# Optimization experiments

Measured on AMD Instinct MI355X. Metric: run time of the kernel, lower is better.

## Reference

```python
import jax, jax.numpy as jnp
import numpy as np

STRIDE = (1, 1)
PAD = 1


def _conv2d(x, w):
    # NCHW conv, OIHW kernel, stride 1, padding 1 (module defaults)
    return jax.lax.conv_general_dilated(
        x, w, window_strides=STRIDE, padding=[(PAD, PAD), (PAD, PAD)],
        dimension_numbers=("NCHW", "OIHW", "NCHW"))


def setup_inputs() -> dict:
    key = jax.random.key(0)
    k1, k2, k3 = jax.random.split(key, 3)
    C, H, W, O, KH, KW = 16, 16, 16, 32, 3, 3
    N = C * H * W  # 4096 flat input features
    base = jax.random.normal(k1, (1, N), dtype=jnp.float32)
    return {
        "x": base,
        "lower_bound": base - 0.1,
        "upper_bound": base + 0.1,
        "input_shape": jnp.array([1, C, H, W], dtype=jnp.int32),
        "kernel": 0.1 * jax.random.normal(k2, (O, C, KH, KW), dtype=jnp.float32),
        "bias": 0.1 * jax.random.normal(k3, (O,), dtype=jnp.float32),
    }


def reference(x, lower_bound, upper_bound, input_shape, kernel, bias):
    shape = tuple(int(s) for s in np.asarray(input_shape))  # (1, C, H, W)
    x4 = x.reshape(shape)
    lb4 = lower_bound.reshape(shape)
    ub4 = upper_bound.reshape(shape)

    # twice inside F.conv2d and once via the explicit reshape-add)
    neg_w = jnp.where(kernel < 0, kernel, 0.0)
    pos_w = jnp.where(kernel >= 0, kernel, 0.0)
    b3 = (3.0 * bias)[None, :, None, None]
    lb_new = _conv2d(ub4, neg_w) + _conv2d(lb4, pos_w) + b3
    ub_new = _conv2d(lb4, neg_w) + _conv2d(ub4, pos_w) + b3
    lb_new = lb_new.reshape(lb_new.shape[0], -1)
    ub_new = ub_new.reshape(ub_new.shape[0], -1)

    # concrete forward through the conv layer (bias once)
    x_out4 = _conv2d(x4, kernel) + bias[None, :, None, None]
    x_out = x_out4.reshape(x_out4.shape[0], -1)

    # unroll conv into an explicit [numel_in, numel_out] matrix.
    # Equivalent to the source's eye().view + conv3d(depth-1 kernel):
    # each basis image is convolved independently -> batched conv2d.
    N = x.shape[1]
    eye_imgs = jnp.eye(N, dtype=kernel.dtype).reshape((N,) + shape[1:])  # [N,C,H,W]
    unrolled = _conv2d(eye_imgs, kernel)  # [N, O, H', W']
    weights = unrolled.reshape(N, -1)     # [numel_in, O*H'*W']
    O_, Hp, Wp = unrolled.shape[1:]
    bias_vec = jnp.broadcast_to(bias[:, None, None], (O_, Hp, Wp)).reshape(-1)

    return (x_out, lb_new, ub_new, weights, bias_vec)
```

## Files before the change

### kernel.cpp

```cpp
#include <hip/hip_runtime.h>

#define O_CH  32
#define C_CH  16
#define HH    16
#define WW    16
#define NPIX  256
#define NIN   4096
#define NOUT  8192
#define NB_WEIGHTS 2048
#define NB_BOUNDS  32

typedef float v4f __attribute__((ext_vector_type(4)));


__global__ __launch_bounds__(256) void fused_deeppoly_kernel(
    const float* __restrict__ x,
    const float* __restrict__ lb,
    const float* __restrict__ ub,
    const float* __restrict__ wk,
    const float* __restrict__ bias,
    float* __restrict__ out) {
    const int b   = blockIdx.x;
    const int tid = threadIdx.x;

    if (b < NB_WEIGHTS) {
        const int colgroup = b & 7;
        const int rowset   = b >> 3;
        const int r   = colgroup * 256 + tid;
        const int o   = r >> 6;
        const int p   = r & 63;
        const int ph  = p >> 2;
        const int pw0 = (p & 3) << 2;
        const int c   = rowset >> 4;
        const int h   = rowset & 15;
        const int kh  = h - ph + 1;

        float k0 = 0.f, k1 = 0.f, k2 = 0.f;
        if ((unsigned)kh < 3u) {
            const float* kb = wk + ((o * C_CH + c) * 3 + kh) * 3;
            k0 = kb[0]; k1 = kb[1]; k2 = kb[2];
        }
        auto sel = [&](int kw) -> float {
            return kw == 0 ? k0 : (kw == 1 ? k1 : (kw == 2 ? k2 : 0.f));
        };

        v4f* wout = (v4f*)(out + 3 * NOUT);
        v4f* pptr = wout + (size_t)(rowset * 16) * 2048 + r;

        v4f v;
        v.x = sel(1 - pw0);
        v.y = sel(-pw0);
        v.z = sel(-1 - pw0);
        v.w = sel(-2 - pw0);
        #pragma unroll
        for (int j = 0; j < 16; ++j) {
            __builtin_nontemporal_store(v, pptr);
            pptr += 2048;
            v.w = v.z; v.z = v.y; v.y = v.x;
            v.x = sel(j + 2 - pw0);
        }
    } else {
        const int o  = b - NB_WEIGHTS;
        const int ph = tid >> 4, pw = tid & 15;
        const float* kb_base = wk + o * C_CH * 9;
        float xa = 0.f, la = 0.f, ua = 0.f;
        #pragma unroll
        for (int c = 0; c < C_CH; ++c) {
            #pragma unroll
            for (int kh = 0; kh < 3; ++kh) {
                int h = ph + kh - 1;
                if ((unsigned)h >= (unsigned)HH) continue;
                #pragma unroll
                for (int kw = 0; kw < 3; ++kw) {
                    int w = pw + kw - 1;
                    if ((unsigned)w >= (unsigned)WW) continue;
                    float k   = kb_base[c * 9 + kh * 3 + kw];
                    int   idx = c * NPIX + h * WW + w;
                    xa = fmaf(k, x[idx], xa);
                    float lv = lb[idx], uv = ub[idx];
                    la = fmaf(k, (k < 0.f) ? uv : lv, la);
                    ua = fmaf(k, (k < 0.f) ? lv : uv, ua);
                }
            }
        }
        const int   t  = o * 256 + tid;
        const float bv = bias[o];
        out[t]            = xa + bv;
        out[NOUT + t]     = la + 3.f * bv;
        out[2 * NOUT + t] = ua + 3.f * bv;
        out[(size_t)3 * NOUT + (size_t)NIN * NOUT + t] = bv;
    }
}

extern "C" void kernel_launch(void* const* d_in, const int* in_sizes, int n_in,
                              void* d_out, int out_size, void* d_ws, size_t ws_size,
                              hipStream_t stream) {
    const float* x    = (const float*)d_in[0];
    const float* lbp  = (const float*)d_in[1];
    const float* ubp  = (const float*)d_in[2];
    const float* wk   = (const float*)d_in[4];
    const float* bias = (const float*)d_in[5];

    fused_deeppoly_kernel<<<NB_WEIGHTS + NB_BOUNDS, 256, 0, stream>>>(
        x, lbp, ubp, wk, bias, (float*)d_out);
}
```

Baseline: 165.4 us.

## Remap weight-matrix writer so each block writes two contiguous output rows

Each weight block now covers two consecutive input rows (a contiguous 64KB span) instead of 16 rows strided by 2048 vectors for one column group. Each thread issues 16 coalesced vector stores of 4096-float rows and reloads kernel taps per output channel. Nontemporal stores are replaced by ordinary stores. The aim is a more sequential DRAM write pattern, at the cost of more kernel-weight loads per thread and possible cache pollution from normal stores.

```diff
diff --git a/kernel.cpp b/kernel.cpp
--- a/kernel.cpp
+++ b/kernel.cpp
@@ -12,7 +12,6 @@
 
 typedef float v4f __attribute__((ext_vector_type(4)));
 
-
 __global__ __launch_bounds__(256) void fused_deeppoly_kernel(
     const float* __restrict__ x,
     const float* __restrict__ lb,
@@ -24,40 +23,40 @@
     const int tid = threadIdx.x;
 
     if (b < NB_WEIGHTS) {
-        const int colgroup = b & 7;
-        const int rowset   = b >> 3;
-        const int r   = colgroup * 256 + tid;
-        const int o   = r >> 6;
-        const int p   = r & 63;
-        const int ph  = p >> 2;
-        const int pw0 = (p & 3) << 2;
-        const int c   = rowset >> 4;
-        const int h   = rowset & 15;
-        const int kh  = h - ph + 1;
+        const int n0   = 2 * b;
+        const int c    = n0 >> 8;
+        const int h    = (n0 >> 4) & 15;
+        const int w0   = n0 & 15;
+        const int ph   = (tid & 63) >> 2;
+        const int pw0  = (tid & 3) << 2;
+        const int osub = tid >> 6;
+        const int kh   = h - ph + 1;
+        const bool kvalid = (unsigned)kh < 3u;
+        const int  khc = kvalid ? kh : 0;
 
-        float k0 = 0.f, k1 = 0.f, k2 = 0.f;
-        if ((unsigned)kh < 3u) {
-            const float* kb = wk + ((o * C_CH + c) * 3 + kh) * 3;
-            k0 = kb[0]; k1 = kb[1]; k2 = kb[2];
-        }
-        auto sel = [&](int kw) -> float {
-            return kw == 0 ? k0 : (kw == 1 ? k1 : (kw == 2 ? k2 : 0.f));
-        };
+        v4f* p = (v4f*)(out + 3 * NOUT) + (size_t)b * 4096 + tid;
 
-        v4f* wout = (v4f*)(out + 3 * NOUT);
-        v4f* pptr = wout + (size_t)(rowset * 16) * 2048 + r;
-
-        v4f v;
-        v.x = sel(1 - pw0);
-        v.y = sel(-pw0);
-        v.z = sel(-1 - pw0);
-        v.w = sel(-2 - pw0);
         #pragma unroll
-        for (int j = 0; j < 16; ++j) {
-            __builtin_nontemporal_store(v, pptr);
-            pptr += 2048;
-            v.w = v.z; v.z = v.y; v.y = v.x;
-            v.x = sel(j + 2 - pw0);
+        for (int half = 0; half < 2; ++half) {
+            const int w   = w0 + half;
+            const int kw0 = w - pw0 + 1;
+            #pragma unroll
+            for (int jj = 0; jj < 8; ++jj) {
+                const int o = jj * 4 + osub;
+                const float* kb = wk + ((o * C_CH + c) * 3 + khc) * 3;
+                float k0 = kb[0], k1 = kb[1], k2 = kb[2];
+                if (!kvalid) { k0 = 0.f; k1 = 0.f; k2 = 0.f; }
+                auto sel = [&](int kw) -> float {
+                    return kw == 0 ? k0 : (kw == 1 ? k1 : (kw == 2 ? k2 : 0.f));
+                };
+                v4f v;
+                v.x = sel(kw0);
+                v.y = sel(kw0 - 1);
+                v.z = sel(kw0 - 2);
+                v.w = sel(kw0 - 3);
+                *p = v;
+                p += 256;
+            }
         }
     } else {
         const int o  = b - NB_WEIGHTS;
```

Measured after the change: 163.5 us. Within noise of the previous version (-1.2%).

## Remap weight-matrix blocks by spatial position and loop over channels with plain stores

Applied to the files above, without the earlier changes.

The unrolled-weight writer now gives each block one (h,w) input position and loops over the 16 channels, each iteration reloading three kernel taps and writing a 16-byte vector with a stride of 524288 vec4s. The old version held one kernel row in registers and shifted it across 16 rows with nontemporal stores. Bounds blocks move to the front of the grid so they are scheduled first. The write pattern per block changes, each block now issues more small kernel loads, and the switch to normal stores may pollute the cache on this large write-only output.

```diff
diff --git a/kernel.cpp b/kernel.cpp
--- a/kernel.cpp
+++ b/kernel.cpp
@@ -7,11 +7,10 @@
 #define NPIX  256
 #define NIN   4096
 #define NOUT  8192
+#define NB_BOUNDS  32
 #define NB_WEIGHTS 2048
-#define NB_BOUNDS  32
 
 typedef float v4f __attribute__((ext_vector_type(4)));
-
 
 __global__ __launch_bounds__(256) void fused_deeppoly_kernel(
     const float* __restrict__ x,
@@ -23,44 +22,43 @@
     const int b   = blockIdx.x;
     const int tid = threadIdx.x;
 
-    if (b < NB_WEIGHTS) {
-        const int colgroup = b & 7;
-        const int rowset   = b >> 3;
-        const int r   = colgroup * 256 + tid;
+    if (b >= NB_BOUNDS) {
+        const int bw  = b - NB_BOUNDS;
+        const int nb  = bw >> 3;
+        const int r   = (bw & 7) * 256 + tid;
         const int o   = r >> 6;
         const int p   = r & 63;
         const int ph  = p >> 2;
         const int pw0 = (p & 3) << 2;
-        const int c   = rowset >> 4;
-        const int h   = rowset & 15;
+        const int h   = nb >> 4;
+        const int w   = nb & 15;
         const int kh  = h - ph + 1;
+        const bool kvalid = (unsigned)kh < 3u;
+        const int  khc = kvalid ? kh : 0;
+        const int  kw0 = w - pw0 + 1;
 
-        float k0 = 0.f, k1 = 0.f, k2 = 0.f;
-        if ((unsigned)kh < 3u) {
-            const float* kb = wk + ((o * C_CH + c) * 3 + kh) * 3;
-            k0 = kb[0]; k1 = kb[1]; k2 = kb[2];
-        }
-        auto sel = [&](int kw) -> float {
-            return kw == 0 ? k0 : (kw == 1 ? k1 : (kw == 2 ? k2 : 0.f));
-        };
+        const bool vx0 = kvalid && kw0 == 0, vx1 = kvalid && kw0 == 1, vx2 = kvalid && kw0 == 2;
+        const bool vy0 = kvalid && kw0 == 1, vy1 = kvalid && kw0 == 2, vy2 = kvalid && kw0 == 3;
+        const bool vz0 = kvalid && kw0 == 2, vz1 = kvalid && kw0 == 3, vz2 = kvalid && kw0 == 4;
+        const bool vw0 = kvalid && kw0 == 3, vw1 = kvalid && kw0 == 4, vw2 = kvalid && kw0 == 5;
 
-        v4f* wout = (v4f*)(out + 3 * NOUT);
-        v4f* pptr = wout + (size_t)(rowset * 16) * 2048 + r;
+        const float* kb = wk + (o * C_CH * 3 + khc) * 3;
+        v4f* p4 = (v4f*)(out + 3 * NOUT) + (size_t)bw * 256 + tid;
 
-        v4f v;
-        v.x = sel(1 - pw0);
-        v.y = sel(-pw0);
-        v.z = sel(-1 - pw0);
-        v.w = sel(-2 - pw0);
         #pragma unroll
-        for (int j = 0; j < 16; ++j) {
-            __builtin_nontemporal_store(v, pptr);
-            pptr += 2048;
-            v.w = v.z; v.z = v.y; v.y = v.x;
-            v.x = sel(j + 2 - pw0);
+        for (int c = 0; c < C_CH; ++c) {
+            const float k0 = kb[0], k1 = kb[1], k2 = kb[2];
+            v4f v;
+            v.x = vx0 ? k0 : (vx1 ? k1 : (vx2 ? k2 : 0.f));
+            v.y = vy0 ? k0 : (vy1 ? k1 : (vy2 ? k2 : 0.f));
+            v.z = vz0 ? k0 : (vz1 ? k1 : (vz2 ? k2 : 0.f));
+            v.w = vw0 ? k0 : (vw1 ? k1 : (vw2 ? k2 : 0.f));
+            *p4 = v;
+            p4 += 524288;
+            kb += 9;
         }
     } else {
-        const int o  = b - NB_WEIGHTS;
+        const int o  = b;
         const int ph = tid >> 4, pw = tid & 15;
         const float* kb_base = wk + o * C_CH * 9;
         float xa = 0.f, la = 0.f, ua = 0.f;
@@ -101,6 +99,6 @@
     const float* wk   = (const float*)d_in[4];
     const float* bias = (const float*)d_in[5];
 
-    fused_deeppoly_kernel<<<NB_WEIGHTS + NB_BOUNDS, 256, 0, stream>>>(
+    fused_deeppoly_kernel<<<NB_BOUNDS + NB_WEIGHTS, 256, 0, stream>>>(
         x, lbp, ubp, wk, bias, (float*)d_out);
 }
```

Measured after the change: 160.0 us, median of 2. 3.3% less time.
